# Performance work log

Measured on AMD Instinct MI355X. Metric: run time of the kernel, lower is better.

The kernel has to match this reference:

```python
import jax, jax.numpy as jnp
import numpy as np

# Model dims (match init_kwargs)
B, S, D = 4, 2048, 1024          # batch, seq, d_model
H, E, DH = 8, 4, 128             # n_heads, n_experts_attn, d_head
K = 2                            # k_attn (routed, n_expert_shared_attn=0)
NEG_INF = jnp.float32(-1e30)


def setup_inputs() -> dict:
    key = jax.random.key(0)
    ks = jax.random.split(key, 9)
    s = np.float32(1.0 / np.sqrt(D))
    return {
        "q_src": jax.random.normal(ks[0], (B, S, D), jnp.float32),
        "k_src": jax.random.normal(ks[1], (B, S, D), jnp.float32),
        "v_src": jax.random.normal(ks[2], (B, S, D), jnp.float32),
        "wq": jax.random.normal(ks[3], (H * DH, D), jnp.float32) * s,
        "wk": jax.random.normal(ks[4], (H * DH, D), jnp.float32) * s,
        "sel_v_w": jax.random.normal(ks[5], (H * E, D), jnp.float32) * s,
        "sel_o_w": jax.random.normal(ks[6], (H * E, D), jnp.float32) * s,
        "v_w": jax.random.normal(ks[7], (H, E, D, DH), jnp.float32) * s,
        "o_w": jax.random.normal(ks[8], (H, E, DH, D), jnp.float32) * np.float32(1.0 / np.sqrt(H * DH)),
        "bias_v": jnp.zeros((E,), jnp.float32),   # load-balancing bias buffer (zeros at init)
        "bias_o": jnp.zeros((E,), jnp.float32),
        # causal boolean mask, True = attend (skip_mask all True -> trimming is identity)
        "attn_mask": jnp.broadcast_to(jnp.tril(jnp.ones((S, S), bool)), (B, S, S)),
        "position_ids": jnp.broadcast_to(jnp.arange(S, dtype=jnp.int32), (B, S)),
        "skip_mask": jnp.ones((B, S), bool),
    }


def _expert_gate(x, w, bias):
    """Sigmoid gating + per-head top-k routed expert selection.
    Returns dense combine weights [b,s,h,E] (sum of sel_val * one_hot) and indices [b,s,h,K]."""
    logits = (x @ w.T).reshape(*x.shape[:-1], H, E)        # [b,s,h,E]
    sel = jax.nn.sigmoid(logits)
    # bias only affects *which* experts are picked (added under no_grad in torch)
    _, idx = jax.lax.top_k(jax.lax.stop_gradient(sel) + bias, K)  # [b,s,h,K]
    sel_val = jnp.take_along_axis(sel, idx, axis=-1)        # [b,s,h,K]
    gate = jnp.sum(jax.nn.one_hot(idx, E, dtype=sel.dtype) * sel_val[..., None], axis=-2)
    return gate, idx


def reference(q_src, k_src, v_src, wq, wk, sel_v_w, sel_o_w, v_w, o_w,
              bias_v, bias_o, attn_mask, position_ids, skip_mask):
    # scale.sqrt() applied to both q and k -> full 1/sqrt(d_head) on scores
    ssq = jnp.float32((1.0 / np.sqrt(DH)) ** 0.5)
    q = ((q_src @ wq.T) * ssq).reshape(B, S, H, DH).transpose(0, 2, 1, 3)  # [b,h,s,dh]
    k = ((k_src @ wk.T) * ssq).reshape(B, S, H, DH).transpose(0, 2, 1, 3)

    v_gate, v_idx = _expert_gate(k_src, sel_v_w, bias_v)    # V experts routed on k_src
    o_gate, o_idx = _expert_gate(q_src, sel_o_w, bias_o)    # O experts routed on q_src

    # expert-mixed V projection (cvmm): all experts then dense combine
    all_v = jnp.einsum('bsm,hemd->bshed', v_src, v_w)       # [b,s,h,E,dh]
    v = jnp.einsum('bshed,bshe->bhsd', all_v, v_gate)       # [b,h,s,dh]

    scores = jnp.einsum('bhqd,bhkd->bhqk', q, k)
    scores = jnp.where(attn_mask[:, None], scores, NEG_INF)
    attn = jax.nn.softmax(scores, axis=-1)
    out = jnp.einsum('bhqk,bhkd->bqhd', attn, v)            # [b,s,h,dh]

    # expert-mixed O projection, summed over heads
    scaled = out[..., None, :] * o_gate[..., None]          # [b,s,h,E,dh]
    res = jnp.einsum('bshed,hedm->bsm', scaled, o_w)        # [b,s,d_model]
    return res, (v_idx, o_idx)
```

## Files before the change

kernel.cpp:

```cpp
#include <hip/hip_runtime.h>
#include <cstdint>
#include <cstddef>

typedef __bf16 bf16;
typedef __bf16 bf16x4 __attribute__((ext_vector_type(4)));
typedef __bf16 bf16x8 __attribute__((ext_vector_type(8)));
typedef float  fx4    __attribute__((ext_vector_type(4)));


__device__ __forceinline__ void async16(const void* g, void* l) {
  __builtin_amdgcn_global_load_lds((const __attribute__((address_space(1))) void*)g,
                                   (__attribute__((address_space(3))) void*)l, 16, 0, 0);
}

#define BARRIER() do { asm volatile("" ::: "memory"); __builtin_amdgcn_s_barrier(); \
                       asm volatile("" ::: "memory"); } while (0)

template <int CTRL>
__device__ __forceinline__ float dppf(float x) {
  return __int_as_float(__builtin_amdgcn_update_dpp(
      0, __float_as_int(x), CTRL, 0xf, 0xf, true));
}

__global__ __launch_bounds__(256) void cvt_all(const float4* __restrict__ q,
                                               const float4* __restrict__ k,
                                               const float4* __restrict__ v,
                                               const float4* __restrict__ wq,
                                               const float4* __restrict__ wk,
                                               bf16x4* __restrict__ qo, bf16x4* __restrict__ ko,
                                               bf16x4* __restrict__ vo, bf16x4* __restrict__ wqo,
                                               bf16x4* __restrict__ wko) {
  const int y = blockIdx.y;
  const float4* s; bf16x4* d; int n4;
  if      (y == 0) { s = q;  d = qo;  n4 = 2097152; }
  else if (y == 1) { s = k;  d = ko;  n4 = 2097152; }
  else if (y == 2) { s = v;  d = vo;  n4 = 2097152; }
  else if (y == 3) { s = wq; d = wqo; n4 = 262144; }
  else             { s = wk; d = wko; n4 = 262144; }
  int i = blockIdx.x * 256 + threadIdx.x;
  if (i < n4) {
    float4 t = s[i];
    bf16x4 o;
    o[0] = (bf16)t.x; o[1] = (bf16)t.y; o[2] = (bf16)t.z; o[3] = (bf16)t.w;
    d[i] = o;
  }
}

__global__ __launch_bounds__(256) void make_w(const float* __restrict__ v_w,
                                              const float* __restrict__ o_w,
                                              bf16* __restrict__ wvt,
                                              bf16* __restrict__ wot) {
  __shared__ float tile[64][65];
  if (blockIdx.z < 32) {
    const int he = blockIdx.z, k0 = blockIdx.x * 64, dh0 = blockIdx.y * 64;
    const float* in = v_w + (size_t)he * 1024 * 128;
    #pragma unroll
    for (int j = 0; j < 16; j++) {
      int idx = threadIdx.x + j * 256;
      int r = idx >> 6, c = idx & 63;
      tile[r][c] = in[(size_t)(k0 + r) * 128 + dh0 + c];
    }
    __syncthreads();
    const int h = he >> 2, e = he & 3;
    bf16* outp = wvt + ((size_t)(h * 128 + dh0) * 4 + e) * 1024 + k0;
    #pragma unroll
    for (int j = 0; j < 16; j++) {
      int idx = threadIdx.x + j * 256;
      int r = idx >> 6, c = idx & 63;
      outp[(size_t)r * 4096 + c] = (bf16)tile[c][r];
    }
  } else {
    const int he = blockIdx.z - 32, d0 = blockIdx.x * 64, dh0 = blockIdx.y * 64;
    const float* in = o_w + (size_t)he * 128 * 1024;
    #pragma unroll
    for (int j = 0; j < 16; j++) {
      int idx = threadIdx.x + j * 256;
      int r = idx >> 6, c = idx & 63;
      tile[r][c] = in[(size_t)(dh0 + r) * 1024 + d0 + c];
    }
    __syncthreads();
    bf16* outp = wot + (size_t)d0 * 4096 + he * 128 + dh0;
    #pragma unroll
    for (int j = 0; j < 16; j++) {
      int idx = threadIdx.x + j * 256;
      int r = idx >> 6, c = idx & 63;
      outp[(size_t)r * 4096 + c] = (bf16)tile[c][r];
    }
  }
}

__global__ __launch_bounds__(256) void gating(const float* __restrict__ q_src,
                                              const float* __restrict__ k_src,
                                              const float* __restrict__ sel_v_w,
                                              const float* __restrict__ sel_o_w,
                                              const float* __restrict__ bias_v,
                                              const float* __restrict__ bias_o,
                                              float* __restrict__ gate_v,
                                              float* __restrict__ gate_o,
                                              float* __restrict__ d_out) {
  const int g = blockIdx.y;
  const int m0 = blockIdx.x * 64;
  const float* x = g ? q_src : k_src;
  const float* w = g ? sel_o_w : sel_v_w;
  const float* bias = g ? bias_o : bias_v;
  float* gate = g ? gate_o : gate_v;
  float* idxo = d_out + 8388608 + g * 131072;

  __shared__ __align__(16) float smem[2 * 12288];

  const int t = threadIdx.x;
  const int hg = t & 7;
  const int tg = t >> 3;

  auto stage = [&](int buf, int k0) {
    float* xs = smem + buf * 12288;
    float* ws = xs + 8192;
    #pragma unroll
    for (int p = 0; p < 8; p++) {
      int of = p * 1024 + t * 4;
      int row = of >> 7, c = (of >> 2) & 31;
      int sc = c ^ ((row >> 1) & 7);
      async16(x + (size_t)(m0 + row) * 1024 + k0 + sc * 4, xs + of);
    }
    #pragma unroll
    for (int p = 0; p < 4; p++) {
      int of = p * 1024 + t * 4;
      int row = of >> 7, c = (of >> 2) & 31;
      int sc = c ^ ((row >> 2) & 7);
      async16(w + (size_t)row * 1024 + k0 + sc * 4, ws + of);
    }
  };

  double acc[2][4] = {};

  stage(0, 0);
  int buf = 0;
  for (int c8 = 0; c8 < 8; c8++) {
    if (c8 < 7) {
      stage(buf ^ 1, (c8 + 1) * 128);
      asm volatile("s_waitcnt vmcnt(12)" ::: "memory");
    } else {
      asm volatile("s_waitcnt vmcnt(0)" ::: "memory");
    }
    BARRIER();
    const float* xs = smem + buf * 12288;
    const float* ws = xs + 8192;
    const int xr0 = tg * 2;
    #pragma unroll 4
    for (int k4 = 0; k4 < 32; k4++) {
      float4 x0 = *(const float4*)(xs + (size_t)xr0 * 128 + (size_t)((k4 ^ (tg & 7)) * 4));
      float4 x1 = *(const float4*)(xs + (size_t)(xr0 + 1) * 128 + (size_t)((k4 ^ (tg & 7)) * 4));
      double x0d[4] = {(double)x0.x, (double)x0.y, (double)x0.z, (double)x0.w};
      double x1d[4] = {(double)x1.x, (double)x1.y, (double)x1.z, (double)x1.w};
      #pragma unroll
      for (int e = 0; e < 4; e++) {
        int wr = hg * 4 + e;
        float4 wv = *(const float4*)(ws + (size_t)wr * 128 + (size_t)((k4 ^ hg) * 4));
        double w0 = (double)wv.x, w1 = (double)wv.y, w2 = (double)wv.z, w3 = (double)wv.w;
        acc[0][e] += x0d[0] * w0 + x0d[1] * w1 + x0d[2] * w2 + x0d[3] * w3;
        acc[1][e] += x1d[0] * w0 + x1d[1] * w1 + x1d[2] * w2 + x1d[3] * w3;
      }
    }
    BARRIER();
    buf ^= 1;
  }

  const float log2e = 1.4426950408889634f;
  float b0 = bias[0], b1 = bias[1], b2 = bias[2], b3 = bias[3];
  #pragma unroll
  for (int tok = 0; tok < 2; tok++) {
    int m = m0 + tg * 2 + tok;
    float sel[4];
    #pragma unroll
    for (int e = 0; e < 4; e++) {
      float lv = (float)acc[tok][e];
      sel[e] = 1.0f / (1.0f + __builtin_amdgcn_exp2f(-lv * log2e));
    }
    float vb[4] = {sel[0] + b0, sel[1] + b1, sel[2] + b2, sel[3] + b3};
    int i0 = 0;
    #pragma unroll
    for (int e = 1; e < 4; e++) if (vb[e] > vb[i0]) i0 = e;
    int i1 = -1; float best = -1e30f;
    #pragma unroll
    for (int e = 0; e < 4; e++) { if (e == i0) continue; if (vb[e] > best) { best = vb[e]; i1 = e; } }
    float4 gv;
    gv.x = (i0 == 0 || i1 == 0) ? sel[0] : 0.f;
    gv.y = (i0 == 1 || i1 == 1) ? sel[1] : 0.f;
    gv.z = (i0 == 2 || i1 == 2) ? sel[2] : 0.f;
    gv.w = (i0 == 3 || i1 == 3) ? sel[3] : 0.f;
    *(float4*)(gate + ((size_t)m * 8 + hg) * 4) = gv;
    idxo[m * 16 + hg * 2 + 0] = (float)i0;
    idxo[m * 16 + hg * 2 + 1] = (float)i1;
  }
}

template <int MODE>
__global__ __launch_bounds__(512) void gemm_moe(const bf16* __restrict__ Abf,
                                                const bf16* __restrict__ BT,
                                                const float* __restrict__ gate,
                                                bf16* __restrict__ Cbf,
                                                float* __restrict__ Cf32,
                                                float scale,
                                                const bf16* __restrict__ Abf2,
                                                const bf16* __restrict__ BT2,
                                                bf16* __restrict__ Cbf2,
                                                float scale2) {
  constexpr int KDIM = (MODE == 0) ? 1024 : 4096;
  constexpr int ASTRIDE = (MODE == 2) ? 4096 : 1024;
  __shared__ __align__(16) bf16 smem[49152];
  const int t = threadIdx.x;
  const int wave = t >> 6, lane = t & 63;
  const int wr = wave >> 1, wc = wave & 1;
  const int quad = lane >> 4, l16 = lane & 15;
  const int bid = blockIdx.x;
  const int sel = (MODE == 0) ? (bid >> 8) : 0;
  const bf16* A  = sel ? Abf2 : Abf;
  const bf16* Bt = sel ? BT2  : BT;
  bf16* Cb       = sel ? Cbf2 : Cbf;
  const float scl = sel ? scale2 : scale;
  const int lbid = (MODE == 0) ? (bid & 255) : bid;
  const int mt = (MODE == 1) ? (lbid >> 3) : (lbid & 31);
  const int np = (MODE == 1) ? (lbid & 7) : (lbid >> 5);
  const int m0 = mt * 256;
  const int n0 = (MODE == 1) ? 0 : np * 128;
  const int h = (MODE == 1) ? np : 0;
  const bf16* BTh = (MODE == 1) ? Bt + (size_t)h * 128 * 4096 : Bt;

  fx4 acc[4][4] = {};
  fx4 accT[4][4] = {};

  const int srow = t >> 3, sch = t & 7;

  auto stage = [&](int buf, int k0) {
    bf16* As = smem + buf * 16384;
    bf16* Bs = smem + 32768 + buf * 8192;
    #pragma unroll
    for (int p = 0; p < 2; p++) {
      int row = p * 64 + srow;
      int sc = sch ^ (row & 7);
      async16(BTh + (size_t)(n0 + row) * KDIM + k0 + sc * 8,
              Bs + row * 64 + sch * 8);
    }
    int col = (MODE == 1) ? (k0 & 1023) : k0;
    #pragma unroll
    for (int p = 0; p < 4; p++) {
      int row = p * 64 + srow;
      int sc = sch ^ (row & 7);
      async16(A + (size_t)(m0 + row) * ASTRIDE + col + sc * 8,
              As + row * 64 + sch * 8);
    }
  };

  stage(0, 0);
  int buf = 0;
  for (int k0 = 0; k0 < KDIM; k0 += 64) {
    if (k0 + 64 < KDIM) {
      stage(buf ^ 1, k0 + 64);
      asm volatile("s_waitcnt vmcnt(6)" ::: "memory");
    } else {
      asm volatile("s_waitcnt vmcnt(0)" ::: "memory");
    }
    BARRIER();
    const bf16* As = smem + buf * 16384;
    const bf16* Bs = smem + 32768 + buf * 8192;
    #pragma unroll
    for (int kk = 0; kk < 64; kk += 32) {
      bf16x8 af[4], bfr[4];
      #pragma unroll
      for (int i = 0; i < 4; i++) {
        int ar = wr * 64 + i * 16 + l16;
        af[i] = *(const bf16x8*)(As + ar * 64 + ((((kk >> 3) + quad) ^ (ar & 7)) * 8));
      }
      #pragma unroll
      for (int i = 0; i < 2; i++) {
        int br = wc * 64 + i * 16 + l16;
        bfr[i] = *(const bf16x8*)(Bs + br * 64 + ((((kk >> 3) + quad) ^ (br & 7)) * 8));
      }
      BARRIER();
      __builtin_amdgcn_s_setprio(1);
      #pragma unroll
      for (int mi = 0; mi < 4; mi++)
        #pragma unroll
        for (int ni = 0; ni < 2; ni++)
          acc[mi][ni] = __builtin_amdgcn_mfma_f32_16x16x32_bf16(af[mi], bfr[ni], acc[mi][ni], 0, 0, 0);
      __builtin_amdgcn_s_setprio(0);
      BARRIER();
      #pragma unroll
      for (int i = 2; i < 4; i++) {
        int br = wc * 64 + i * 16 + l16;
        bfr[i] = *(const bf16x8*)(Bs + br * 64 + ((((kk >> 3) + quad) ^ (br & 7)) * 8));
      }
      BARRIER();
      __builtin_amdgcn_s_setprio(1);
      #pragma unroll
      for (int mi = 0; mi < 4; mi++)
        #pragma unroll
        for (int ni = 2; ni < 4; ni++)
          acc[mi][ni] = __builtin_amdgcn_mfma_f32_16x16x32_bf16(af[mi], bfr[ni], acc[mi][ni], 0, 0, 0);
      __builtin_amdgcn_s_setprio(0);
      BARRIER();
    }
    if constexpr (MODE == 1) {
      if (((k0 + 64) & 1023) == 0) {
        const int e = k0 >> 10;
        #pragma unroll
        for (int mi = 0; mi < 4; mi++)
          #pragma unroll
          for (int r = 0; r < 4; r++) {
            int m = m0 + wr * 64 + mi * 16 + quad * 4 + r;
            float gv = gate[((size_t)m * 8 + h) * 4 + e];
            #pragma unroll
            for (int ni = 0; ni < 4; ni++)
              accT[mi][ni][r] += gv * acc[mi][ni][r];
          }
        #pragma unroll
        for (int mi = 0; mi < 4; mi++)
          #pragma unroll
          for (int ni = 0; ni < 4; ni++)
            #pragma unroll
            for (int j = 0; j < 4; j++) acc[mi][ni][j] = 0.f;
      }
    }
    buf ^= 1;
  }

  if (MODE == 1) {
    #pragma unroll
    for (int mi = 0; mi < 4; mi++)
      #pragma unroll
      for (int ni = 0; ni < 4; ni++) {
        int nl = wc * 64 + ni * 16 + l16;
        int ml = wr * 64 + mi * 16 + quad * 4;
        bf16x4 pk;
        #pragma unroll
        for (int r = 0; r < 4; r++) pk[r] = (bf16)accT[mi][ni][r];
        *(bf16x4*)(smem + nl * 264 + ml) = pk;
      }
    __syncthreads();
    int b = m0 >> 11, s0 = m0 & 2047;
    const int row = t >> 2, seg = t & 3;
    bf16* dst = Cb + (((size_t)(b * 8 + h) * 128) + row) * 2048 + s0 + seg * 64;
    #pragma unroll
    for (int j = 0; j < 8; j++)
      *(float4*)(dst + j * 8) = *(float4*)(smem + row * 264 + seg * 64 + j * 8);
    return;
  }

  #pragma unroll
  for (int mi = 0; mi < 4; mi++)
    #pragma unroll
    for (int ni = 0; ni < 4; ni++)
      #pragma unroll
      for (int r = 0; r < 4; r++) {
        int m = m0 + wr * 64 + mi * 16 + quad * 4 + r;
        int n = n0 + wc * 64 + ni * 16 + l16;
        float v = acc[mi][ni][r] * scl;
        if (MODE == 0) {
          int b = m >> 11, s = m & 2047, hh = n >> 7, dh = n & 127;
          Cb[(((size_t)(b * 8 + hh) * 2048 + s) << 7) + dh] = (bf16)v;
        } else {
          Cf32[(size_t)m * 1024 + n] = v;
        }
      }
}

__global__ __launch_bounds__(256) void attn_kernel(const bf16* __restrict__ qb,
                                                   const bf16* __restrict__ kb,
                                                   const bf16* __restrict__ vbT,
                                                   const float* __restrict__ gate_o,
                                                   bf16* __restrict__ Ae) {
  const int linear = blockIdx.y * 16 + blockIdx.x;
  const int bh = (linear & 7) * 4 + ((linear >> 3) & 3);
  const int px = linear >> 5;
  const int b = bh >> 3, h = bh & 7;
  __shared__ __align__(16) bf16 Ks[2][64 * 128];
  __shared__ __align__(16) bf16 VTs[2][128 * 64];
  __shared__ __align__(16) bf16 Ps[4][16][72];
  const int t = threadIdx.x, wave = t >> 6, lane = t & 63;
  const int quad = lane >> 4, l16 = lane & 15;
  const bf16* qbase  = qb  + (size_t)bh * 2048 * 128;
  const bf16* kbase  = kb  + (size_t)bh * 2048 * 128;
  const bf16* vtbase = vbT + (size_t)bh * 128 * 2048;

  auto stage = [&](int buf, int kt) {
    #pragma unroll
    for (int p = 0; p < 4; p++) {
      int o = p * 4096 + wave * 1024 + lane * 16;
      int kr = o >> 8, kc = o & 255;
      async16((const char*)kbase + (size_t)(kt * 64 + kr) * 256 + (kc ^ ((kr & 7) << 4)),
              (char*)&Ks[buf][0] + o);
    }
    #pragma unroll
    for (int p = 0; p < 4; p++) {
      int o = p * 4096 + wave * 1024 + lane * 16;
      int vr = o >> 7, vc = o & 127;
      async16((const char*)vtbase + (size_t)vr * 4096 + kt * 128 + (vc ^ ((vr & 7) << 4)),
              (char*)&VTs[buf][0] + o);
    }
  };

  #pragma unroll 1
  for (int pass = 0; pass < 2; pass++) {
    const int qt = pass ? px : (31 - px);

    bf16x8 qf[4];
    #pragma unroll
    for (int dk = 0; dk < 4; dk++)
      qf[dk] = *(const bf16x8*)(qbase + (size_t)(qt * 64 + wave * 16 + l16) * 128 + dk * 32 + quad * 8);

    float m_run[4], l_run[4];
    fx4 acc_o[8] = {};
    #pragma unroll
    for (int r = 0; r < 4; r++) { m_run[r] = -1e30f; l_run[r] = 0.f; }

    stage(0, 0);
    int cur = 0;

    for (int kt = 0; kt <= qt; kt++) {
      if (kt < qt) {
        stage(cur ^ 1, kt + 1);
        asm volatile("s_waitcnt vmcnt(8)" ::: "memory");
      } else {
        asm volatile("s_waitcnt vmcnt(0)" ::: "memory");
      }
      __builtin_amdgcn_s_barrier();
      asm volatile("" ::: "memory");

      const char* Ksb  = (const char*)&Ks[cur][0];
      const char* VTsb = (const char*)&VTs[cur][0];

      fx4 accs[4] = {};
      __builtin_amdgcn_s_setprio(1);
      #pragma unroll
      for (int ni = 0; ni < 4; ni++)
        #pragma unroll
        for (int dk = 0; dk < 4; dk++) {
          int r = ni * 16 + l16;
          bf16x8 kf = *(const bf16x8*)(Ksb + r * 256 + ((dk * 64 + quad * 16) ^ ((r & 7) << 4)));
          accs[ni] = __builtin_amdgcn_mfma_f32_16x16x32_bf16(qf[dk], kf, accs[ni], 0, 0, 0);
        }
      __builtin_amdgcn_s_setprio(0);

      if (kt == qt) {
        #pragma unroll
        for (int ni = 0; ni < 4; ni++)
          #pragma unroll
          for (int r = 0; r < 4; r++) {
            int qr = wave * 16 + quad * 4 + r;
            int kc = ni * 16 + l16;
            if (kc > qr) accs[ni][r] = -1e30f;
          }
      }

      float mxv[4];
      #pragma unroll
      for (int r = 0; r < 4; r++) {
        float mx = fmaxf(fmaxf(accs[0][r], accs[1][r]), fmaxf(accs[2][r], accs[3][r]));
        mx = fmaxf(mx, dppf<0x121>(mx));
        mx = fmaxf(mx, dppf<0x122>(mx));
        mx = fmaxf(mx, dppf<0x124>(mx));
        mx = fmaxf(mx, dppf<0x128>(mx));
        mxv[r] = mx;
      }
      bool defer = (mxv[0] <= m_run[0] + 8.f) && (mxv[1] <= m_run[1] + 8.f) &&
                   (mxv[2] <= m_run[2] + 8.f) && (mxv[3] <= m_run[3] + 8.f);
      if (__all(defer)) {
        #pragma unroll
        for (int r = 0; r < 4; r++) {
          float rs = 0.f;
          #pragma unroll
          for (int ni = 0; ni < 4; ni++) {
            float p = __builtin_amdgcn_exp2f(accs[ni][r] - m_run[r]);
            accs[ni][r] = p; rs += p;
          }
          rs += dppf<0x121>(rs);
          rs += dppf<0x122>(rs);
          rs += dppf<0x124>(rs);
          rs += dppf<0x128>(rs);
          l_run[r] += rs;
        }
      } else {
        #pragma unroll
        for (int r = 0; r < 4; r++) {
          float m_new = fmaxf(m_run[r], mxv[r]);
          float alpha = __builtin_amdgcn_exp2f(m_run[r] - m_new);
          float rs = 0.f;
          #pragma unroll
          for (int ni = 0; ni < 4; ni++) {
            float p = __builtin_amdgcn_exp2f(accs[ni][r] - m_new);
            accs[ni][r] = p; rs += p;
          }
          rs += dppf<0x121>(rs);
          rs += dppf<0x122>(rs);
          rs += dppf<0x124>(rs);
          rs += dppf<0x128>(rs);
          l_run[r] = l_run[r] * alpha + rs;
          m_run[r] = m_new;
          #pragma unroll
          for (int nj = 0; nj < 8; nj++) acc_o[nj][r] *= alpha;
        }
      }

      #pragma unroll
      for (int ni = 0; ni < 4; ni++)
        #pragma unroll
        for (int r = 0; r < 4; r++)
          Ps[wave][quad * 4 + r][ni * 16 + l16] = (bf16)accs[ni][r];

      __builtin_amdgcn_s_setprio(1);
      #pragma unroll
      for (int step = 0; step < 2; step++) {
        bf16x8 pf = *(const bf16x8*)&Ps[wave][l16][step * 32 + quad * 8];
        #pragma unroll
        for (int nj = 0; nj < 8; nj++) {
          int r = nj * 16 + l16;
          bf16x8 vf = *(const bf16x8*)(VTsb + r * 128 + ((step * 64 + quad * 16) ^ ((r & 7) << 4)));
          acc_o[nj] = __builtin_amdgcn_mfma_f32_16x16x32_bf16(pf, vf, acc_o[nj], 0, 0, 0);
        }
      }
      __builtin_amdgcn_s_setprio(0);

      asm volatile("" ::: "memory");
      __builtin_amdgcn_s_barrier();
      cur ^= 1;
    }

    #pragma unroll
    for (int r = 0; r < 4; r++) {
      int s = qt * 64 + wave * 16 + quad * 4 + r;
      int token = b * 2048 + s;
      float4 g4 = *(const float4*)(gate_o + ((size_t)token * 8 + h) * 4);
      float inv = 1.0f / l_run[r];
      #pragma unroll
      for (int nj = 0; nj < 8; nj++) {
        float o = acc_o[nj][r] * inv;
        bf16* dst = Ae + (size_t)token * 4096 + (h * 4) * 128 + nj * 16 + l16;
        dst[0]   = (bf16)(o * g4.x);
        dst[128] = (bf16)(o * g4.y);
        dst[256] = (bf16)(o * g4.z);
        dst[384] = (bf16)(o * g4.w);
      }
    }
  }
}

extern "C" void kernel_launch(void* const* d_in, const int* in_sizes, int n_in,
                              void* d_out, int out_size, void* d_ws, size_t ws_size,
                              hipStream_t stream) {
  const float* q_src  = (const float*)d_in[0];
  const float* k_src  = (const float*)d_in[1];
  const float* v_src  = (const float*)d_in[2];
  const float* wq     = (const float*)d_in[3];
  const float* wk     = (const float*)d_in[4];
  const float* sel_v_w = (const float*)d_in[5];
  const float* sel_o_w = (const float*)d_in[6];
  const float* v_w    = (const float*)d_in[7];
  const float* o_w    = (const float*)d_in[8];
  const float* bias_v = (const float*)d_in[9];
  const float* bias_o = (const float*)d_in[10];
  float* out = (float*)d_out;

  char* ws = (char*)d_ws;
  size_t off = 0;
  auto alloc = [&](size_t bytes) { char* p = ws + off; off += (bytes + 255) & ~(size_t)255; return p; };
  bf16* wqb   = (bf16*)alloc((size_t)1024 * 1024 * 2);
  bf16* wkb   = (bf16*)alloc((size_t)1024 * 1024 * 2);
  bf16* wvt   = (bf16*)alloc((size_t)8 * 128 * 4 * 1024 * 2);
  bf16* wot   = (bf16*)alloc((size_t)1024 * 4096 * 2);
  float* gate_v = (float*)alloc((size_t)8192 * 32 * 4);
  float* gate_o = (float*)alloc((size_t)8192 * 32 * 4);
  bf16* qsb   = (bf16*)alloc((size_t)8192 * 1024 * 2);
  bf16* ksb   = (bf16*)alloc((size_t)8192 * 1024 * 2);
  bf16* vsb   = (bf16*)alloc((size_t)8192 * 1024 * 2);
  (void)alloc((size_t)8192 * 1024 * 2);
  bf16* Ae    = qsb;
  bf16* qb    = (bf16*)alloc((size_t)8192 * 1024 * 2);
  bf16* kb    = (bf16*)alloc((size_t)8192 * 1024 * 2);
  bf16* vbT   = (bf16*)alloc((size_t)8192 * 1024 * 2);

  cvt_all<<<dim3(8192, 5), 256, 0, stream>>>((const float4*)q_src, (const float4*)k_src,
                                             (const float4*)v_src, (const float4*)wq,
                                             (const float4*)wk, (bf16x4*)qsb, (bf16x4*)ksb,
                                             (bf16x4*)vsb, (bf16x4*)wqb, (bf16x4*)wkb);
  make_w<<<dim3(16, 2, 64), 256, 0, stream>>>(v_w, o_w, wvt, wot);
  gating<<<dim3(128, 2), 256, 0, stream>>>(q_src, k_src, sel_v_w, sel_o_w,
                                           bias_v, bias_o, gate_v, gate_o, out);

  const float ssq = 0.29730177875068026f;
  const float log2e = 1.4426950408889634f;
  gemm_moe<0><<<512, 512, 0, stream>>>(qsb, wqb, nullptr, qb, nullptr, ssq * log2e,
                                       ksb, wkb, kb, ssq);
  gemm_moe<1><<<256, 512, 0, stream>>>(vsb, wvt, gate_v, vbT, nullptr, 1.0f,
                                       nullptr, nullptr, nullptr, 0.f);
  attn_kernel<<<dim3(16, 32), 256, 0, stream>>>(qb, kb, vbT, gate_o, Ae);
  gemm_moe<2><<<256, 512, 0, stream>>>(Ae, wot, nullptr, nullptr, out, 1.0f,
                                       nullptr, nullptr, nullptr, 0.f);
}
```

Before: 561.6 us.

## Enlarge attention Q tile to 128 rows per block with single-buffered V

Each attention block now processes one 128-row query tile, 32 rows per wave, instead of two paired 64-row tiles, and drops the heavy/light causal pairing in favour of largest-tile-first ordering. Each K and V tile loaded into LDS is reused by twice as many MFMAs, which cuts global and LDS traffic per FLOP. V is single-buffered and its prefetch is issued after the second barrier, and the P scratch gains an XOR swizzle to reduce bank conflicts. In exchange, each wave uses more registers for two sets of accumulators, load balance across blocks is less even, and the V load is exposed until the next iteration.

```diff
diff --git a/kernel.cpp b/kernel.cpp
--- a/kernel.cpp
+++ b/kernel.cpp
@@ -371,18 +371,19 @@
                                                    bf16* __restrict__ Ae) {
   const int linear = blockIdx.y * 16 + blockIdx.x;
   const int bh = (linear & 7) * 4 + ((linear >> 3) & 3);
-  const int px = linear >> 5;
+  const int qt = 15 - (linear >> 5);
   const int b = bh >> 3, h = bh & 7;
+  const int n_kv = 2 * qt + 2;
   __shared__ __align__(16) bf16 Ks[2][64 * 128];
-  __shared__ __align__(16) bf16 VTs[2][128 * 64];
-  __shared__ __align__(16) bf16 Ps[4][16][72];
+  __shared__ __align__(16) bf16 VTs[128 * 64];
+  __shared__ __align__(16) bf16 Ps[4][32 * 64];
   const int t = threadIdx.x, wave = t >> 6, lane = t & 63;
   const int quad = lane >> 4, l16 = lane & 15;
   const bf16* qbase  = qb  + (size_t)bh * 2048 * 128;
   const bf16* kbase  = kb  + (size_t)bh * 2048 * 128;
   const bf16* vtbase = vbT + (size_t)bh * 128 * 2048;
 
-  auto stage = [&](int buf, int kt) {
+  auto stageK = [&](int buf, int kt) {
     #pragma unroll
     for (int p = 0; p < 4; p++) {
       int o = p * 4096 + wave * 1024 + lane * 16;
@@ -390,150 +391,178 @@
       async16((const char*)kbase + (size_t)(kt * 64 + kr) * 256 + (kc ^ ((kr & 7) << 4)),
               (char*)&Ks[buf][0] + o);
     }
+  };
+  auto stageV = [&](int kt) {
     #pragma unroll
     for (int p = 0; p < 4; p++) {
       int o = p * 4096 + wave * 1024 + lane * 16;
       int vr = o >> 7, vc = o & 127;
       async16((const char*)vtbase + (size_t)vr * 4096 + kt * 128 + (vc ^ ((vr & 7) << 4)),
-              (char*)&VTs[buf][0] + o);
+              (char*)&VTs[0] + o);
     }
   };
 
-  #pragma unroll 1
-  for (int pass = 0; pass < 2; pass++) {
-    const int qt = pass ? px : (31 - px);
-
-    bf16x8 qf[4];
+  bf16x8 qf[2][4];
+  #pragma unroll
+  for (int g = 0; g < 2; g++)
     #pragma unroll
     for (int dk = 0; dk < 4; dk++)
-      qf[dk] = *(const bf16x8*)(qbase + (size_t)(qt * 64 + wave * 16 + l16) * 128 + dk * 32 + quad * 8);
-
-    float m_run[4], l_run[4];
-    fx4 acc_o[8] = {};
-    #pragma unroll
-    for (int r = 0; r < 4; r++) { m_run[r] = -1e30f; l_run[r] = 0.f; }
-
-    stage(0, 0);
-    int cur = 0;
-
-    for (int kt = 0; kt <= qt; kt++) {
-      if (kt < qt) {
-        stage(cur ^ 1, kt + 1);
-        asm volatile("s_waitcnt vmcnt(8)" ::: "memory");
-      } else {
-        asm volatile("s_waitcnt vmcnt(0)" ::: "memory");
-      }
-      __builtin_amdgcn_s_barrier();
-      asm volatile("" ::: "memory");
-
-      const char* Ksb  = (const char*)&Ks[cur][0];
-      const char* VTsb = (const char*)&VTs[cur][0];
-
-      fx4 accs[4] = {};
-      __builtin_amdgcn_s_setprio(1);
-      #pragma unroll
-      for (int ni = 0; ni < 4; ni++)
-        #pragma unroll
-        for (int dk = 0; dk < 4; dk++) {
-          int r = ni * 16 + l16;
-          bf16x8 kf = *(const bf16x8*)(Ksb + r * 256 + ((dk * 64 + quad * 16) ^ ((r & 7) << 4)));
-          accs[ni] = __builtin_amdgcn_mfma_f32_16x16x32_bf16(qf[dk], kf, accs[ni], 0, 0, 0);
-        }
-      __builtin_amdgcn_s_setprio(0);
-
-      if (kt == qt) {
+      qf[g][dk] = *(const bf16x8*)(qbase +
+          (size_t)(qt * 128 + wave * 32 + g * 16 + l16) * 128 + dk * 32 + quad * 8);
+
+  float m_run[2][4], l_run[2][4];
+  fx4 acc_o[2][8] = {};
+  #pragma unroll
+  for (int g = 0; g < 2; g++)
+    #pragma unroll
+    for (int r = 0; r < 4; r++) { m_run[g][r] = -1e30f; l_run[g][r] = 0.f; }
+
+  stageK(0, 0);
+  stageV(0);
+  int cur = 0;
+
+  for (int kt = 0; kt < n_kv; kt++) {
+    if (kt + 1 < n_kv) {
+      stageK(cur ^ 1, kt + 1);
+      asm volatile("s_waitcnt vmcnt(4)" ::: "memory");
+    } else {
+      asm volatile("s_waitcnt vmcnt(0)" ::: "memory");
+    }
+    __builtin_amdgcn_s_barrier();
+    asm volatile("" ::: "memory");
+
+    const char* Ksb = (const char*)&Ks[cur][0];
+
+    fx4 accs[2][4] = {};
+    __builtin_amdgcn_s_setprio(1);
+    #pragma unroll
+    for (int ni = 0; ni < 4; ni++)
+      #pragma unroll
+      for (int dk = 0; dk < 4; dk++) {
+        int r = ni * 16 + l16;
+        bf16x8 kf = *(const bf16x8*)(Ksb + r * 256 + ((dk * 64 + quad * 16) ^ ((r & 7) << 4)));
+        accs[0][ni] = __builtin_amdgcn_mfma_f32_16x16x32_bf16(qf[0][dk], kf, accs[0][ni], 0, 0, 0);
+        accs[1][ni] = __builtin_amdgcn_mfma_f32_16x16x32_bf16(qf[1][dk], kf, accs[1][ni], 0, 0, 0);
+      }
+    __builtin_amdgcn_s_setprio(0);
+
+    if (kt >= n_kv - 2) {
+      #pragma unroll
+      for (int g = 0; g < 2; g++)
         #pragma unroll
         for (int ni = 0; ni < 4; ni++)
           #pragma unroll
           for (int r = 0; r < 4; r++) {
-            int qr = wave * 16 + quad * 4 + r;
-            int kc = ni * 16 + l16;
-            if (kc > qr) accs[ni][r] = -1e30f;
+            int qg = qt * 128 + wave * 32 + g * 16 + quad * 4 + r;
+            int kg = kt * 64 + ni * 16 + l16;
+            if (kg > qg) accs[g][ni][r] = -1e30f;
           }
-      }
-
-      float mxv[4];
+    }
+
+    float mxv[2][4];
+    #pragma unroll
+    for (int g = 0; g < 2; g++)
       #pragma unroll
       for (int r = 0; r < 4; r++) {
-        float mx = fmaxf(fmaxf(accs[0][r], accs[1][r]), fmaxf(accs[2][r], accs[3][r]));
+        float mx = fmaxf(fmaxf(accs[g][0][r], accs[g][1][r]),
+                         fmaxf(accs[g][2][r], accs[g][3][r]));
         mx = fmaxf(mx, dppf<0x121>(mx));
         mx = fmaxf(mx, dppf<0x122>(mx));
         mx = fmaxf(mx, dppf<0x124>(mx));
         mx = fmaxf(mx, dppf<0x128>(mx));
-        mxv[r] = mx;
-      }
-      bool defer = (mxv[0] <= m_run[0] + 8.f) && (mxv[1] <= m_run[1] + 8.f) &&
-                   (mxv[2] <= m_run[2] + 8.f) && (mxv[3] <= m_run[3] + 8.f);
-      if (__all(defer)) {
+        mxv[g][r] = mx;
+      }
+    bool defer = true;
+    #pragma unroll
+    for (int g = 0; g < 2; g++)
+      #pragma unroll
+      for (int r = 0; r < 4; r++) defer = defer && (mxv[g][r] <= m_run[g][r] + 8.f);
+    if (__all(defer)) {
+      #pragma unroll
+      for (int g = 0; g < 2; g++)
         #pragma unroll
         for (int r = 0; r < 4; r++) {
           float rs = 0.f;
           #pragma unroll
           for (int ni = 0; ni < 4; ni++) {
-            float p = __builtin_amdgcn_exp2f(accs[ni][r] - m_run[r]);
-            accs[ni][r] = p; rs += p;
+            float p = __builtin_amdgcn_exp2f(accs[g][ni][r] - m_run[g][r]);
+            accs[g][ni][r] = p; rs += p;
           }
           rs += dppf<0x121>(rs);
           rs += dppf<0x122>(rs);
           rs += dppf<0x124>(rs);
           rs += dppf<0x128>(rs);
-          l_run[r] += rs;
+          l_run[g][r] += rs;
         }
-      } else {
+    } else {
+      #pragma unroll
+      for (int g = 0; g < 2; g++)
         #pragma unroll
         for (int r = 0; r < 4; r++) {
-          float m_new = fmaxf(m_run[r], mxv[r]);
-          float alpha = __builtin_amdgcn_exp2f(m_run[r] - m_new);
+          float m_new = fmaxf(m_run[g][r], mxv[g][r]);
+          float alpha = __builtin_amdgcn_exp2f(m_run[g][r] - m_new);
           float rs = 0.f;
           #pragma unroll
           for (int ni = 0; ni < 4; ni++) {
-            float p = __builtin_amdgcn_exp2f(accs[ni][r] - m_new);
-            accs[ni][r] = p; rs += p;
+            float p = __builtin_amdgcn_exp2f(accs[g][ni][r] - m_new);
+            accs[g][ni][r] = p; rs += p;
           }
           rs += dppf<0x121>(rs);
           rs += dppf<0x122>(rs);
           rs += dppf<0x124>(rs);
           rs += dppf<0x128>(rs);
-          l_run[r] = l_run[r] * alpha + rs;
-          m_run[r] = m_new;
+          l_run[g][r] = l_run[g][r] * alpha + rs;
+          m_run[g][r] = m_new;
           #pragma unroll
-          for (int nj = 0; nj < 8; nj++) acc_o[nj][r] *= alpha;
+          for (int nj = 0; nj < 8; nj++) acc_o[g][nj][r] *= alpha;
         }
-      }
-
+    }
+
+    #pragma unroll
+    for (int g = 0; g < 2; g++)
       #pragma unroll
       for (int ni = 0; ni < 4; ni++)
         #pragma unroll
-        for (int r = 0; r < 4; r++)
-          Ps[wave][quad * 4 + r][ni * 16 + l16] = (bf16)accs[ni][r];
-
-      __builtin_amdgcn_s_setprio(1);
-      #pragma unroll
-      for (int step = 0; step < 2; step++) {
-        bf16x8 pf = *(const bf16x8*)&Ps[wave][l16][step * 32 + quad * 8];
-        #pragma unroll
-        for (int nj = 0; nj < 8; nj++) {
-          int r = nj * 16 + l16;
-          bf16x8 vf = *(const bf16x8*)(VTsb + r * 128 + ((step * 64 + quad * 16) ^ ((r & 7) << 4)));
-          acc_o[nj] = __builtin_amdgcn_mfma_f32_16x16x32_bf16(pf, vf, acc_o[nj], 0, 0, 0);
+        for (int r = 0; r < 4; r++) {
+          int row = g * 16 + quad * 4 + r;
+          int byo = row * 128 + (((ni * 16 + l16) * 2) ^ ((row & 7) << 4));
+          *(bf16*)((char*)&Ps[wave][0] + byo) = (bf16)accs[g][ni][r];
         }
-      }
-      __builtin_amdgcn_s_setprio(0);
-
-      asm volatile("" ::: "memory");
-      __builtin_amdgcn_s_barrier();
-      cur ^= 1;
-    }
-
+
+    __builtin_amdgcn_s_setprio(1);
+    #pragma unroll
+    for (int step = 0; step < 2; step++) {
+      int swz = (step * 64 + quad * 16) ^ ((l16 & 7) << 4);
+      bf16x8 pf0 = *(const bf16x8*)((const char*)&Ps[wave][0] + l16 * 128 + swz);
+      bf16x8 pf1 = *(const bf16x8*)((const char*)&Ps[wave][0] + (16 + l16) * 128 + swz);
+      #pragma unroll
+      for (int nj = 0; nj < 8; nj++) {
+        int r = nj * 16 + l16;
+        bf16x8 vf = *(const bf16x8*)((const char*)&VTs[0] + r * 128 +
+                                     ((step * 64 + quad * 16) ^ ((r & 7) << 4)));
+        acc_o[0][nj] = __builtin_amdgcn_mfma_f32_16x16x32_bf16(pf0, vf, acc_o[0][nj], 0, 0, 0);
+        acc_o[1][nj] = __builtin_amdgcn_mfma_f32_16x16x32_bf16(pf1, vf, acc_o[1][nj], 0, 0, 0);
+      }
+    }
+    __builtin_amdgcn_s_setprio(0);
+
+    asm volatile("" ::: "memory");
+    __builtin_amdgcn_s_barrier();
+    if (kt + 1 < n_kv) stageV(kt + 1);
+    cur ^= 1;
+  }
+
+  #pragma unroll
+  for (int g = 0; g < 2; g++)
     #pragma unroll
     for (int r = 0; r < 4; r++) {
-      int s = qt * 64 + wave * 16 + quad * 4 + r;
+      int s = qt * 128 + wave * 32 + g * 16 + quad * 4 + r;
       int token = b * 2048 + s;
       float4 g4 = *(const float4*)(gate_o + ((size_t)token * 8 + h) * 4);
-      float inv = 1.0f / l_run[r];
+      float inv = 1.0f / l_run[g][r];
       #pragma unroll
       for (int nj = 0; nj < 8; nj++) {
-        float o = acc_o[nj][r] * inv;
+        float o = acc_o[g][nj][r] * inv;
         bf16* dst = Ae + (size_t)token * 4096 + (h * 4) * 128 + nj * 16 + l16;
         dst[0]   = (bf16)(o * g4.x);
         dst[128] = (bf16)(o * g4.y);
@@ -541,7 +570,6 @@
         dst[384] = (bf16)(o * g4.w);
       }
     }
-  }
 }
 
 extern "C" void kernel_launch(void* const* d_in, const int* in_sizes, int n_in,
```

Result: slower. 583.9 us (+4.0%).
